# Kernel tuning notes

Measured on AMD Instinct MI355X. Metric: run time of the kernel, lower is better.

## Reference

```python
import jax, jax.numpy as jnp
import numpy as np

G, T, D_IN, D_OUT = 8, 8192, 1024, 1024
# fixed uneven per-expert token counts summing to T (variable-size groups)
_COUNTS = np.array([512, 1536, 1024, 1024, 768, 1280, 896, 1152], dtype=np.int32)
assert _COUNTS.sum() == T


def setup_inputs() -> dict:
    key = jax.random.key(0)
    k1, k2 = jax.random.split(key)
    hidden_states = jax.random.normal(k1, (T, D_IN), dtype=jnp.float32)
    # kaiming_uniform_(a=sqrt(5)) on [G, in, out] -> bound = sqrt(3/ (fan_in)) with gain sqrt(1/3)
    bound = 1.0 / np.sqrt(D_IN)
    weight = jax.random.uniform(k2, (G, D_IN, D_OUT), dtype=jnp.float32, minval=-bound, maxval=bound)
    tokens_per_expert = jnp.asarray(_COUNTS)
    return {"hidden_states": hidden_states, "weight": weight, "tokens_per_expert": tokens_per_expert}


def reference(hidden_states, weight, tokens_per_expert):
    # grouped GEMM: token t in group g (per contiguous split by tokens_per_expert)
    # gets out[t] = hidden_states[t] @ weight[g]
    T_ = hidden_states.shape[0]
    G_ = weight.shape[0]
    offsets = jnp.cumsum(tokens_per_expert)  # [G] end offsets of each group
    expert_id = jnp.searchsorted(offsets, jnp.arange(T_), side="right")  # [T]
    out = jnp.zeros((T_, weight.shape[2]), dtype=hidden_states.dtype)
    for g in range(G_):  # small fixed expert count; masked accumulate keeps shapes static
        mask = (expert_id == g).astype(hidden_states.dtype)[:, None]
        out = out + mask * (hidden_states @ weight[g])
    return out
```

## Files before the change

kernel.cpp:

```cpp
#include <hip/hip_runtime.h>
#include <hip/hip_bf16.h>

typedef __attribute__((ext_vector_type(8))) short short8;
typedef __attribute__((ext_vector_type(4))) float f32x4;

constexpr int Tt = 8192, Kd = 1024, Nd = 1024, Gn = 8;
constexpr int BM = 128, BN = 128, BK = 64;
constexpr int NKT = Kd / BK;

static __device__ __forceinline__ short f2bf(float x) {
    __hip_bfloat16 b = __float2bfloat16(x);
    return *reinterpret_cast<short*>(&b);
}

__global__ __launch_bounds__(256, 2)
void grouped_gemm_kernel(const float* __restrict__ H,
                         const float* __restrict__ W,
                         const int* __restrict__ counts,
                         float* __restrict__ out)
{
    __shared__ __align__(16) short As[2][BM * BK];
    __shared__ __align__(16) short Bs[2][BN * BK];

    const int tid = threadIdx.x;
    const int bid = blockIdx.x;
    const int wg = (bid & 7) * 64 + (bid >> 3);
    const int mt = wg >> 3, nt = wg & 7;
    const int row0 = mt * BM, col0 = nt * BN;

    int g = 0;
    {
        int c = 0;
        for (int i = 0; i < Gn; ++i) { c += counts[i]; if (row0 >= c) g = i + 1; }
    }
    const float* __restrict__ Wg = W + (size_t)g * Kd * Nd;

    const int wid = tid >> 6, lane = tid & 63;
    const int wm = wid >> 1, wn = wid & 1;
    const int l15 = lane & 15, l4 = lane >> 4;

    f32x4 acc[4][4];
#pragma unroll
    for (int i = 0; i < 4; ++i)
#pragma unroll
        for (int j = 0; j < 4; ++j) acc[i][j] = (f32x4)0.0f;

    f32x4 a_reg[4][2];
    float b_reg[4][8];

    auto issue_loads = [&](int kt) {
        const int kbase = kt * BK;
#pragma unroll
        for (int i = 0; i < 4; ++i) {
            const int idx = i * 256 + tid;
            const int m = idx >> 3, kc = idx & 7;
            const float* p = H + (size_t)(row0 + m) * Kd + kbase + kc * 8;
            a_reg[i][0] = *(const f32x4*)p;
            a_reg[i][1] = *(const f32x4*)(p + 4);
        }
#pragma unroll
        for (int i = 0; i < 4; ++i) {
            const int idx = i * 256 + tid;
            const int kc = idx >> 7, n = idx & 127;
            const float* p = Wg + (size_t)(kbase + kc * 8) * Nd + col0 + n;
#pragma unroll
            for (int j = 0; j < 8; ++j) b_reg[i][j] = p[(size_t)j * Nd];
        }
    };

    auto write_stage = [&](int buf) {
#pragma unroll
        for (int i = 0; i < 4; ++i) {
            const int idx = i * 256 + tid;
            const int m = idx >> 3, kc = idx & 7;
            short8 v;
#pragma unroll
            for (int j = 0; j < 4; ++j) v[j] = f2bf(a_reg[i][0][j]);
#pragma unroll
            for (int j = 0; j < 4; ++j) v[4 + j] = f2bf(a_reg[i][1][j]);
            *(short8*)&As[buf][m * BK + ((kc ^ (m & 7)) << 3)] = v;
        }
#pragma unroll
        for (int i = 0; i < 4; ++i) {
            const int idx = i * 256 + tid;
            const int kc = idx >> 7, n = idx & 127;
            short8 v;
#pragma unroll
            for (int j = 0; j < 8; ++j) v[j] = f2bf(b_reg[i][j]);
            *(short8*)&Bs[buf][n * BK + ((kc ^ (n & 7)) << 3)] = v;
        }
    };

    auto compute = [&](int buf) {
#pragma unroll
        for (int ks = 0; ks < 2; ++ks) {
            short8 af[4], bfr[4];
#pragma unroll
            for (int mi = 0; mi < 4; ++mi) {
                const int r = wm * 64 + mi * 16 + l15;
                const int c = (ks * 4 + l4) ^ (r & 7);
                af[mi] = *(const short8*)&As[buf][r * BK + (c << 3)];
            }
#pragma unroll
            for (int ni = 0; ni < 4; ++ni) {
                const int r = wn * 64 + ni * 16 + l15;
                const int c = (ks * 4 + l4) ^ (r & 7);
                bfr[ni] = *(const short8*)&Bs[buf][r * BK + (c << 3)];
            }
#pragma unroll
            for (int mi = 0; mi < 4; ++mi)
#pragma unroll
                for (int ni = 0; ni < 4; ++ni)
                    acc[mi][ni] = __builtin_amdgcn_mfma_f32_16x16x32_bf16(
                        af[mi], bfr[ni], acc[mi][ni], 0, 0, 0);
        }
    };

    issue_loads(0);
    write_stage(0);
    __syncthreads();

    int cur = 0;
    for (int kt = 0; kt < NKT; ++kt) {
        if (kt + 1 < NKT) issue_loads(kt + 1);
        compute(cur);
        if (kt + 1 < NKT) write_stage(cur ^ 1);
        __syncthreads();
        cur ^= 1;
    }

#pragma unroll
    for (int mi = 0; mi < 4; ++mi) {
        const int rbase = row0 + wm * 64 + mi * 16 + l4 * 4;
#pragma unroll
        for (int ni = 0; ni < 4; ++ni) {
            const int c = col0 + wn * 64 + ni * 16 + l15;
#pragma unroll
            for (int r = 0; r < 4; ++r)
                out[(size_t)(rbase + r) * Nd + c] = acc[mi][ni][r];
        }
    }
}

extern "C" void kernel_launch(void* const* d_in, const int* in_sizes, int n_in,
                              void* d_out, int out_size, void* d_ws, size_t ws_size,
                              hipStream_t stream) {
    const float* H = (const float*)d_in[0];
    const float* W = (const float*)d_in[1];
    const int* counts = (const int*)d_in[2];
    float* out = (float*)d_out;
    const int grid = (Tt / BM) * (Nd / BN);
    grouped_gemm_kernel<<<grid, 256, 0, stream>>>(H, W, counts, out);
}
```

Before: 39.50 us.

## Stage A tile via direct global-to-LDS loads in fp32, halve BK

Loads the activation tile straight from global memory into shared memory as fp32 using global_load_lds, with an XOR swizzle applied on the source address. Conversion to bf16 now happens when fragments are read from LDS, which frees the registers that used to stage A. BK drops to 32 so the fp32 A buffer fits, and launch bounds ask for 3 blocks per CU. In exchange there are twice as many K iterations and barriers, conversion work moves into the compute loop and is repeated by every warp that reads a row, and the W tile is still loaded with strided scalar reads through registers.

New measurement: 48.13 us. 1.22x slower.

```diff
diff --git a/kernel.cpp b/kernel.cpp
--- a/kernel.cpp
+++ b/kernel.cpp
@@ -1,11 +1,12 @@
 #include <hip/hip_runtime.h>
 #include <hip/hip_bf16.h>
+#include <stdint.h>
 
 typedef __attribute__((ext_vector_type(8))) short short8;
 typedef __attribute__((ext_vector_type(4))) float f32x4;
 
 constexpr int Tt = 8192, Kd = 1024, Nd = 1024, Gn = 8;
-constexpr int BM = 128, BN = 128, BK = 64;
+constexpr int BM = 128, BN = 128, BK = 32;
 constexpr int NKT = Kd / BK;
 
 static __device__ __forceinline__ short f2bf(float x) {
@@ -13,14 +14,14 @@
     return *reinterpret_cast<short*>(&b);
 }
 
-__global__ __launch_bounds__(256, 2)
+__global__ __launch_bounds__(256, 3)
 void grouped_gemm_kernel(const float* __restrict__ H,
                          const float* __restrict__ W,
                          const int* __restrict__ counts,
                          float* __restrict__ out)
 {
-    __shared__ __align__(16) short As[2][BM * BK];
-    __shared__ __align__(16) short Bs[2][BN * BK];
+    __shared__ __align__(16) float Asf[2][BM * BK];
+    __shared__ __align__(16) short Bss[2][BN * BK];
 
     const int tid = threadIdx.x;
     const int bid = blockIdx.x;
@@ -45,88 +46,78 @@
 #pragma unroll
         for (int j = 0; j < 4; ++j) acc[i][j] = (f32x4)0.0f;
 
-    f32x4 a_reg[4][2];
-    float b_reg[4][8];
+    float breg[16];
+    const int bn = tid & 127, bkh = tid >> 7;
 
-    auto issue_loads = [&](int kt) {
+    auto stage_a = [&](int kt, int buf) {
         const int kbase = kt * BK;
 #pragma unroll
         for (int i = 0; i < 4; ++i) {
-            const int idx = i * 256 + tid;
-            const int m = idx >> 3, kc = idx & 7;
-            const float* p = H + (size_t)(row0 + m) * Kd + kbase + kc * 8;
-            a_reg[i][0] = *(const f32x4*)p;
-            a_reg[i][1] = *(const f32x4*)(p + 4);
-        }
-#pragma unroll
-        for (int i = 0; i < 4; ++i) {
-            const int idx = i * 256 + tid;
-            const int kc = idx >> 7, n = idx & 127;
-            const float* p = Wg + (size_t)(kbase + kc * 8) * Nd + col0 + n;
-#pragma unroll
-            for (int j = 0; j < 8; ++j) b_reg[i][j] = p[(size_t)j * Nd];
+            const int q = wid * 4 + i;
+            const int d = q * 64 + lane;
+            const int m = d >> 3, gc = d & 7;
+            const float* src = H + (size_t)(row0 + m) * Kd + kbase + ((gc ^ (m & 7)) << 2);
+            __builtin_amdgcn_global_load_lds(
+                (const __attribute__((address_space(1))) uint32_t*)src,
+                (__attribute__((address_space(3))) uint32_t*)(&Asf[buf][q * 256]),
+                16, 0, 0);
         }
     };
 
-    auto write_stage = [&](int buf) {
+    auto load_b = [&](int kt) {
+        const float* p = Wg + (size_t)(kt * BK + bkh * 16) * Nd + col0 + bn;
 #pragma unroll
-        for (int i = 0; i < 4; ++i) {
-            const int idx = i * 256 + tid;
-            const int m = idx >> 3, kc = idx & 7;
-            short8 v;
+        for (int j = 0; j < 16; ++j) breg[j] = p[(size_t)j * Nd];
+    };
+
+    auto write_b = [&](int buf) {
+        short8 v0, v1;
 #pragma unroll
-            for (int j = 0; j < 4; ++j) v[j] = f2bf(a_reg[i][0][j]);
-#pragma unroll
-            for (int j = 0; j < 4; ++j) v[4 + j] = f2bf(a_reg[i][1][j]);
-            *(short8*)&As[buf][m * BK + ((kc ^ (m & 7)) << 3)] = v;
-        }
-#pragma unroll
-        for (int i = 0; i < 4; ++i) {
-            const int idx = i * 256 + tid;
-            const int kc = idx >> 7, n = idx & 127;
-            short8 v;
-#pragma unroll
-            for (int j = 0; j < 8; ++j) v[j] = f2bf(b_reg[i][j]);
-            *(short8*)&Bs[buf][n * BK + ((kc ^ (n & 7)) << 3)] = v;
-        }
+        for (int j = 0; j < 8; ++j) { v0[j] = f2bf(breg[j]); v1[j] = f2bf(breg[8 + j]); }
+        const int g0 = (bkh * 2) ^ (bn & 3), g1 = (bkh * 2 + 1) ^ (bn & 3);
+        *(short8*)&Bss[buf][bn * 32 + g0 * 8] = v0;
+        *(short8*)&Bss[buf][bn * 32 + g1 * 8] = v1;
     };
 
     auto compute = [&](int buf) {
+        short8 af[4], bf[4];
 #pragma unroll
-        for (int ks = 0; ks < 2; ++ks) {
-            short8 af[4], bfr[4];
+        for (int mi = 0; mi < 4; ++mi) {
+            const int m = wm * 64 + mi * 16 + l15;
+            const int s = m & 7;
+            const f32x4 x0 = *(const f32x4*)&Asf[buf][m * 32 + (((l4 * 2) ^ s) << 2)];
+            const f32x4 x1 = *(const f32x4*)&Asf[buf][m * 32 + (((l4 * 2 + 1) ^ s) << 2)];
+            short8 v;
 #pragma unroll
-            for (int mi = 0; mi < 4; ++mi) {
-                const int r = wm * 64 + mi * 16 + l15;
-                const int c = (ks * 4 + l4) ^ (r & 7);
-                af[mi] = *(const short8*)&As[buf][r * BK + (c << 3)];
-            }
+            for (int j = 0; j < 4; ++j) { v[j] = f2bf(x0[j]); v[4 + j] = f2bf(x1[j]); }
+            af[mi] = v;
+        }
 #pragma unroll
-            for (int ni = 0; ni < 4; ++ni) {
-                const int r = wn * 64 + ni * 16 + l15;
-                const int c = (ks * 4 + l4) ^ (r & 7);
-                bfr[ni] = *(const short8*)&Bs[buf][r * BK + (c << 3)];
-            }
+        for (int ni = 0; ni < 4; ++ni) {
+            const int n = wn * 64 + ni * 16 + l15;
+            bf[ni] = *(const short8*)&Bss[buf][n * 32 + ((l4 ^ (n & 3)) << 3)];
+        }
 #pragma unroll
-            for (int mi = 0; mi < 4; ++mi)
+        for (int mi = 0; mi < 4; ++mi)
 #pragma unroll
-                for (int ni = 0; ni < 4; ++ni)
-                    acc[mi][ni] = __builtin_amdgcn_mfma_f32_16x16x32_bf16(
-                        af[mi], bfr[ni], acc[mi][ni], 0, 0, 0);
-        }
+            for (int ni = 0; ni < 4; ++ni)
+                acc[mi][ni] = __builtin_amdgcn_mfma_f32_16x16x32_bf16(
+                    af[mi], bf[ni], acc[mi][ni], 0, 0, 0);
     };
 
-    issue_loads(0);
-    write_stage(0);
+    stage_a(0, 0);
+    load_b(0);
+    write_b(0);
     __syncthreads();
 
-    int cur = 0;
+    int buf = 0;
     for (int kt = 0; kt < NKT; ++kt) {
-        if (kt + 1 < NKT) issue_loads(kt + 1);
-        compute(cur);
-        if (kt + 1 < NKT) write_stage(cur ^ 1);
+        const bool more = (kt + 1 < NKT);
+        if (more) { stage_a(kt + 1, buf ^ 1); load_b(kt + 1); }
+        compute(buf);
+        if (more) write_b(buf ^ 1);
         __syncthreads();
-        cur ^= 1;
+        buf ^= 1;
     }
 
 #pragma unroll
```
